# Performance work log

Measured on AMD Instinct MI355X. Metric: run time of the kernel, lower is better.

The kernel has to match this reference:

```python
import jax, jax.numpy as jnp
import numpy as np

# Module config (init_kwargs)
OUT_H, OUT_W = 7, 7
SPATIAL_SCALE = 0.25
SAMPLE_NUM = 2          # fixed sampling grid (sample_num > 0 branch of mmcv kernel)
ALIGNED = True
CLOCKWISE = False

B, C, H, W = 2, 256, 200, 200
R = 1000


def setup_inputs() -> dict:
    key = jax.random.key(0)
    k1, k2, k3, k4, k5, k6 = jax.random.split(key, 6)
    features = jax.random.normal(k1, (B, C, H, W), dtype=jnp.float32)
    # rois: (batch_index, cx, cy, w, h, angle) in input-image coordinates
    bidx = jax.random.randint(k2, (R,), 0, B).astype(jnp.float32)
    cx = jax.random.uniform(k3, (R,), minval=100.0, maxval=700.0)
    cy = jax.random.uniform(k4, (R,), minval=100.0, maxval=700.0)
    wh = jax.random.uniform(k5, (R, 2), minval=20.0, maxval=200.0)
    ang = jax.random.uniform(k6, (R,), minval=-np.pi, maxval=np.pi)
    rois = jnp.concatenate(
        [bidx[:, None], cx[:, None], cy[:, None], wh, ang[:, None]], axis=1
    ).astype(jnp.float32)
    return {"features": features, "rois": rois}


def _bilinear_gather(features, bidx, y, x):
    """features: [B,C,H,W]; bidx: [R] int; y,x: [R,P] float. Returns [R,P,C]."""
    Hf, Wf = features.shape[2], features.shape[3]
    valid = (y > -1.0) & (y < Hf) & (x > -1.0) & (x < Wf)
    y = jnp.maximum(y, 0.0)
    x = jnp.maximum(x, 0.0)
    yl = jnp.floor(y).astype(jnp.int32)
    xl = jnp.floor(x).astype(jnp.int32)
    ych = yl >= Hf - 1
    xch = xl >= Wf - 1
    yl = jnp.where(ych, Hf - 1, yl)
    yh = jnp.where(ych, Hf - 1, yl + 1)
    xl = jnp.where(xch, Wf - 1, xl)
    xh = jnp.where(xch, Wf - 1, xl + 1)
    ly = jnp.where(ych, 0.0, y - yl.astype(y.dtype))
    lx = jnp.where(xch, 0.0, x - xl.astype(x.dtype))
    hy, hx = 1.0 - ly, 1.0 - lx
    b = bidx[:, None]  # [R,1] broadcast against [R,P]
    v1 = features[b, :, yl, xl]  # [R,P,C]
    v2 = features[b, :, yl, xh]
    v3 = features[b, :, yh, xl]
    v4 = features[b, :, yh, xh]
    val = (hy * hx)[..., None] * v1 + (hy * lx)[..., None] * v2 \
        + (ly * hx)[..., None] * v3 + (ly * lx)[..., None] * v4
    return jnp.where(valid[..., None], val, 0.0)


def _roi_align_rotated(features, rois):
    g = SAMPLE_NUM
    offset = 0.5 if ALIGNED else 0.0
    bidx = rois[:, 0].astype(jnp.int32)
    cx = rois[:, 1] * SPATIAL_SCALE - offset
    cy = rois[:, 2] * SPATIAL_SCALE - offset
    rw = rois[:, 3] * SPATIAL_SCALE
    rh = rois[:, 4] * SPATIAL_SCALE
    theta = -rois[:, 5] if CLOCKWISE else rois[:, 5]
    if not ALIGNED:
        rw = jnp.maximum(rw, 1.0)
        rh = jnp.maximum(rh, 1.0)
    bin_h = rh / OUT_H
    bin_w = rw / OUT_W
    # sample offsets within roi frame, origin at roi center
    ph = jnp.arange(OUT_H, dtype=jnp.float32)
    pw = jnp.arange(OUT_W, dtype=jnp.float32)
    ig = (jnp.arange(g, dtype=jnp.float32) + 0.5) / g
    # yy: [R, OUT_H, g]; xx: [R, OUT_W, g]
    yy = -rh[:, None, None] / 2.0 + (ph[None, :, None] + ig[None, None, :]) * bin_h[:, None, None]
    xx = -rw[:, None, None] / 2.0 + (pw[None, :, None] + ig[None, None, :]) * bin_w[:, None, None]
    # broadcast to [R, OUT_H, OUT_W, g, g]
    yy5 = yy[:, :, None, :, None]
    xx5 = xx[:, None, :, None, :]
    sin_t = jnp.sin(theta)[:, None, None, None, None]
    cos_t = jnp.cos(theta)[:, None, None, None, None]
    x = yy5 * sin_t + xx5 * cos_t + cx[:, None, None, None, None]
    y = yy5 * cos_t - xx5 * sin_t + cy[:, None, None, None, None]
    P = OUT_H * OUT_W * g * g
    vals = _bilinear_gather(features, bidx, y.reshape(R, P), x.reshape(R, P))  # [R,P,C]
    vals = vals.reshape(R, OUT_H, OUT_W, g * g, C).mean(axis=3)  # [R,OUT_H,OUT_W,C]
    return jnp.transpose(vals, (0, 3, 1, 2))  # [R,C,OUT_H,OUT_W]


def reference(features, rois):
    return _roi_align_rotated(features, rois)
```

## Files before the change

kernel.cpp:

```cpp
#include <hip/hip_runtime.h>
#include <math.h>

#define OUT_H 7
#define OUT_W 7
#define GS 2
#define NBINS (OUT_H * OUT_W)
#define NSAMP (GS * GS)
#define NMETA (NBINS * NSAMP)
#define SPATIAL_SCALE 0.25f
#define B_ 2
#define C_ 256
#define H_ 200
#define W_ 200
#define R_ 1000
#define HW_ (H_ * W_)
#define NBH 25

typedef _Float16 half_t;
typedef __attribute__((ext_vector_type(4))) _Float16 half4;
typedef __attribute__((ext_vector_type(2))) _Float16 half2_t;


__global__ __launch_bounds__(256)
void nchw_to_nhwc_h(const float* __restrict__ in, half_t* __restrict__ out,
                    const float* __restrict__ rois, int* __restrict__ perm) {
    __shared__ float tile[64][65];

    __shared__ int cnt[8];
    __shared__ int novf, take;
    __shared__ unsigned char claimed[R_];
    __shared__ short ovf[R_];
    if (blockIdx.x == 0 && blockIdx.y == 0 && blockIdx.z == 0) {
        const int t0 = threadIdx.x;
        if (t0 < 8) cnt[t0] = 0;
        if (t0 == 0) { novf = 0; take = 0; }
        for (int t = t0; t < R_; t += 256) claimed[t] = 0;
        __syncthreads();
        for (int t = t0; t < R_; t += 256) {
            const float* roi = rois + t * 6;
            int   b   = (int)roi[0];
            float cyf = roi[2] * SPATIAL_SCALE;
            int q = (int)((cyf - 25.0f) * (4.0f / 150.0f));
            q = q < 0 ? 0 : (q > 3 ? 3 : q);
            int band = b * 4 + q;
            band = band < 0 ? 0 : (band > 7 ? 7 : band);
            int rank = atomicAdd(&cnt[band], 1);
            if (rank < R_ / 8) {
                int id = band + 8 * rank;
                perm[id] = t;
                claimed[id] = 1;
            } else {
                ovf[atomicAdd(&novf, 1)] = (short)t;
            }
        }
        __syncthreads();
        for (int t = t0; t < R_; t += 256) {
            if (!claimed[t]) perm[t] = (int)ovf[atomicAdd(&take, 1)];
        }
    }

    const int hw0 = blockIdx.x * 64;
    const int c0  = blockIdx.y * 64;
    const int b   = blockIdx.z;

    {
        const int tx = threadIdx.x & 63;
        const int ty = threadIdx.x >> 6;
        const float* ip = in + ((size_t)b * C_ + c0) * HW_ + hw0;
#pragma unroll
        for (int k = 0; k < 16; ++k)
            tile[ty + 4 * k][tx] = ip[(size_t)(ty + 4 * k) * HW_ + tx];
    }
    __syncthreads();
    {
        const int cp = threadIdx.x & 31;
        const int hr = threadIdx.x >> 5;
        half_t* op = out + ((size_t)b * HW_ + hw0) * C_ + c0;
#pragma unroll
        for (int k = 0; k < 8; ++k) {
            const int hw = hr + 8 * k;
            half2_t h;
            h[0] = (half_t)tile[2 * cp + 0][hw];
            h[1] = (half_t)tile[2 * cp + 1][hw];
            ((half2_t*)(op + (size_t)hw * C_))[cp] = h;
        }
    }
}

template<int B0, int NB>
__device__ __forceinline__ void gather_pass(
        const half4* __restrict__ fp,
        const int4* __restrict__ s_o, const float4* __restrict__ s_w,
        int wave, int lane, int tid,
        float (&obuf)[4][64][NBH], float* __restrict__ out_r) {

    for (int j = wave; j < NB; j += 8) {
        const int m = (B0 + j) * NSAMP;
        float ax = 0.0f, ay = 0.0f, az = 0.0f, aw = 0.0f;

#pragma unroll
        for (int sp = 0; sp < 2; ++sp) {
            const int4   oA = s_o[m + 2 * sp + 0];
            const int4   oB = s_o[m + 2 * sp + 1];
            const float4 wA = s_w[m + 2 * sp + 0];
            const float4 wB = s_w[m + 2 * sp + 1];

            const half4 vA0 = fp[oA.x + lane];
            const half4 vA1 = fp[oA.y + lane];
            const half4 vA2 = fp[oA.z + lane];
            const half4 vA3 = fp[oA.w + lane];
            const half4 vB0 = fp[oB.x + lane];
            const half4 vB1 = fp[oB.y + lane];
            const half4 vB2 = fp[oB.z + lane];
            const half4 vB3 = fp[oB.w + lane];

            ax = fmaf((float)vA0[0], wA.x, ax);
            ay = fmaf((float)vA0[1], wA.x, ay);
            az = fmaf((float)vA0[2], wA.x, az);
            aw = fmaf((float)vA0[3], wA.x, aw);
            ax = fmaf((float)vA1[0], wA.y, ax);
            ay = fmaf((float)vA1[1], wA.y, ay);
            az = fmaf((float)vA1[2], wA.y, az);
            aw = fmaf((float)vA1[3], wA.y, aw);
            ax = fmaf((float)vA2[0], wA.z, ax);
            ay = fmaf((float)vA2[1], wA.z, ay);
            az = fmaf((float)vA2[2], wA.z, az);
            aw = fmaf((float)vA2[3], wA.z, aw);
            ax = fmaf((float)vA3[0], wA.w, ax);
            ay = fmaf((float)vA3[1], wA.w, ay);
            az = fmaf((float)vA3[2], wA.w, az);
            aw = fmaf((float)vA3[3], wA.w, aw);

            ax = fmaf((float)vB0[0], wB.x, ax);
            ay = fmaf((float)vB0[1], wB.x, ay);
            az = fmaf((float)vB0[2], wB.x, az);
            aw = fmaf((float)vB0[3], wB.x, aw);
            ax = fmaf((float)vB1[0], wB.y, ax);
            ay = fmaf((float)vB1[1], wB.y, ay);
            az = fmaf((float)vB1[2], wB.y, az);
            aw = fmaf((float)vB1[3], wB.y, aw);
            ax = fmaf((float)vB2[0], wB.z, ax);
            ay = fmaf((float)vB2[1], wB.z, ay);
            az = fmaf((float)vB2[2], wB.z, az);
            aw = fmaf((float)vB2[3], wB.z, aw);
            ax = fmaf((float)vB3[0], wB.w, ax);
            ay = fmaf((float)vB3[1], wB.w, ay);
            az = fmaf((float)vB3[2], wB.w, az);
            aw = fmaf((float)vB3[3], wB.w, aw);
        }

        obuf[0][lane][j] = ax;
        obuf[1][lane][j] = ay;
        obuf[2][lane][j] = az;
        obuf[3][lane][j] = aw;
    }
    __syncthreads();

    const int E = C_ * NB;
#pragma unroll
    for (int i = 0; i < (E + 511) / 512; ++i) {
        const int e = tid + 512 * i;
        if (e < E) {
            const int c = e / NB;
            const int j = e - c * NB;
            out_r[(size_t)c * NBINS + B0 + j] = obuf[c & 3][c >> 2][j];
        }
    }
    __syncthreads();
}

__global__ __launch_bounds__(512, 8)
void gather_nhwc(const half_t* __restrict__ nhwc,
                 const float* __restrict__ rois,
                 const int* __restrict__ perm,
                 float* __restrict__ out) {
    __shared__ float obuf[4][64][NBH];
    __shared__ int4   s_o[NMETA];
    __shared__ float4 s_w[NMETA];

    const int r    = perm[blockIdx.x];
    const int tid  = threadIdx.x;
    const int wave = tid >> 6;
    const int lane = tid & 63;

    if (tid < NMETA) {
        const float* roi = rois + r * 6;
        const int   b     = (int)roi[0];
        const float cx    = roi[1] * SPATIAL_SCALE - 0.5f;
        const float cy    = roi[2] * SPATIAL_SCALE - 0.5f;
        const float rw    = roi[3] * SPATIAL_SCALE;
        const float rh    = roi[4] * SPATIAL_SCALE;
        const float theta = roi[5];
        const float bin_h = rh * (1.0f / OUT_H);
        const float bin_w = rw * (1.0f / OUT_W);
        float st, ct;
        __sincosf(theta, &st, &ct);

        const int bin = tid >> 2;
        const int s   = tid & 3;
        const int ph  = bin / OUT_W, pw = bin % OUT_W;
        const int iy  = s >> 1,      ix = s & 1;

        const float yy = -rh * 0.5f + ((float)ph + ((float)iy + 0.5f) * 0.5f) * bin_h;
        const float xx = -rw * 0.5f + ((float)pw + ((float)ix + 0.5f) * 0.5f) * bin_w;
        float x = yy * st + xx * ct + cx;
        float y = yy * ct - xx * st + cy;

        const bool valid = (y > -1.0f) && (y < (float)H_) &&
                           (x > -1.0f) && (x < (float)W_);
        y = fmaxf(y, 0.0f);
        x = fmaxf(x, 0.0f);
        int yl = (int)y, xl = (int)x;
        int yh; float ly;
        if (yl >= H_ - 1) { yl = H_ - 1; yh = H_ - 1; ly = 0.0f; }
        else              { yh = yl + 1; ly = y - (float)yl; }
        int xh; float lx;
        if (xl >= W_ - 1) { xl = W_ - 1; xh = W_ - 1; lx = 0.0f; }
        else              { xh = xl + 1; lx = x - (float)xl; }
        const float hy = 1.0f - ly, hx = 1.0f - lx;
        const float scale = valid ? (1.0f / NSAMP) : 0.0f;

        const int bplane = b * HW_;
        s_o[tid] = make_int4((bplane + yl * W_ + xl) * (C_ / 4),
                             (bplane + yl * W_ + xh) * (C_ / 4),
                             (bplane + yh * W_ + xl) * (C_ / 4),
                             (bplane + yh * W_ + xh) * (C_ / 4));
        s_w[tid] = make_float4(hy * hx * scale, hy * lx * scale,
                               ly * hx * scale, ly * lx * scale);
    }
    __syncthreads();

    const half4* __restrict__ fp = (const half4*)nhwc;
    float* out_r = out + (size_t)r * (C_ * NBINS);

    gather_pass< 0, 25>(fp, s_o, s_w, wave, lane, tid, obuf, out_r);
    gather_pass<25, 24>(fp, s_o, s_w, wave, lane, tid, obuf, out_r);
}


struct alignas(16) Samp {
    int o0, o1, o2, o3;
    float w0, w1, w2, w3;
};

__device__ __forceinline__ Samp compute_samp(const float* __restrict__ rois,
                                             int r, int ph, int pw, int s) {
    const float* roi = rois + r * 6;
    int   b     = (int)roi[0];
    float cx    = roi[1] * SPATIAL_SCALE - 0.5f;
    float cy    = roi[2] * SPATIAL_SCALE - 0.5f;
    float rw    = roi[3] * SPATIAL_SCALE;
    float rh    = roi[4] * SPATIAL_SCALE;
    float theta = roi[5];
    float bin_h = rh * (1.0f / OUT_H);
    float bin_w = rw * (1.0f / OUT_W);
    int iy = s / GS, ix = s % GS;
    float yy = -rh * 0.5f + ((float)ph + ((float)iy + 0.5f) * (1.0f / GS)) * bin_h;
    float xx = -rw * 0.5f + ((float)pw + ((float)ix + 0.5f) * (1.0f / GS)) * bin_w;
    float st = sinf(theta), ct = cosf(theta);
    float x = yy * st + xx * ct + cx;
    float y = yy * ct - xx * st + cy;
    bool valid = (y > -1.0f) && (y < (float)H_) && (x > -1.0f) && (x < (float)W_);
    y = fmaxf(y, 0.0f);
    x = fmaxf(x, 0.0f);
    int yl = (int)y;
    int xl = (int)x;
    int yh; float ly;
    if (yl >= H_ - 1) { yl = H_ - 1; yh = H_ - 1; ly = 0.0f; }
    else              { yh = yl + 1; ly = y - (float)yl; }
    int xh; float lx;
    if (xl >= W_ - 1) { xl = W_ - 1; xh = W_ - 1; lx = 0.0f; }
    else              { xh = xl + 1; lx = x - (float)xl; }
    float hy = 1.0f - ly, hx = 1.0f - lx;
    float scale = valid ? (1.0f / NSAMP) : 0.0f;
    Samp sp;
    int base = b * (C_ * H_ * W_);
    sp.o0 = base + yl * W_ + xl;
    sp.o1 = base + yl * W_ + xh;
    sp.o2 = base + yh * W_ + xl;
    sp.o3 = base + yh * W_ + xh;
    sp.w0 = hy * hx * scale;
    sp.w1 = hy * lx * scale;
    sp.w2 = ly * hx * scale;
    sp.w3 = ly * lx * scale;
    return sp;
}

__global__ __launch_bounds__(256)
void mono_kernel(const float* __restrict__ feat,
                 const float* __restrict__ rois,
                 float* __restrict__ out) {
    int tid = blockIdx.x * blockDim.x + threadIdx.x;
    if (tid >= R_ * C_ * NBINS) return;
    int bin = tid % NBINS;
    int rc  = tid / NBINS;
    int c   = rc % C_;
    int r   = rc / C_;
    int coff = c * (H_ * W_);
    float acc = 0.0f;
#pragma unroll
    for (int s = 0; s < NSAMP; ++s) {
        Samp t = compute_samp(rois, r, bin / OUT_W, bin % OUT_W, s);
        acc += t.w0 * feat[coff + t.o0];
        acc += t.w1 * feat[coff + t.o1];
        acc += t.w2 * feat[coff + t.o2];
        acc += t.w3 * feat[coff + t.o3];
    }
    out[tid] = acc;
}


extern "C" void kernel_launch(void* const* d_in, const int* in_sizes, int n_in,
                              void* d_out, int out_size, void* d_ws, size_t ws_size,
                              hipStream_t stream) {
    const float* feat = (const float*)d_in[0];
    const float* rois = (const float*)d_in[1];
    float* out = (float*)d_out;

    const size_t nhwc_bytes = (size_t)B_ * C_ * HW_ * sizeof(half_t);
    const size_t perm_bytes = (size_t)R_ * sizeof(int);

    if (ws_size >= nhwc_bytes + perm_bytes) {
        half_t* nhwc = (half_t*)d_ws;
        int*    perm = (int*)((char*)d_ws + nhwc_bytes);
        dim3 tgrid(HW_ / 64, C_ / 64, B_);
        nchw_to_nhwc_h<<<tgrid, 256, 0, stream>>>(feat, nhwc, rois, perm);
        gather_nhwc<<<R_, 512, 0, stream>>>(nhwc, rois, perm, out);
    } else {
        const int n_out = R_ * C_ * NBINS;
        mono_kernel<<<(n_out + 255) / 256, 256, 0, stream>>>(feat, rois, out);
    }
}
```

Baseline: 178.3 us.

## Split ROI gather into quarter blocks, use fma_mix, vectorize and swizzle transpose

The gather kernel now launches four 256-thread blocks per ROI, each covering 12 or 13 output bins, in place of one 512-thread block running two passes. This gives more and smaller blocks for scheduling. The inner accumulation uses inline v_fma_mix_f32 to multiply fp16 pairs directly into fp32 accumulators, with all 16 loads issued up front. The NCHW-to-NHWC transpose switches to 128-bit nontemporal loads, an XOR-swizzled shared tile, and 16-byte half8 stores. These changes add inline-asm dependence and recompute per-ROI metadata four times.

```diff
diff --git a/kernel.cpp b/kernel.cpp
--- a/kernel.cpp
+++ b/kernel.cpp
@@ -6,7 +6,6 @@
 #define GS 2
 #define NBINS (OUT_H * OUT_W)
 #define NSAMP (GS * GS)
-#define NMETA (NBINS * NSAMP)
 #define SPATIAL_SCALE 0.25f
 #define B_ 2
 #define C_ 256
@@ -14,17 +13,18 @@
 #define W_ 200
 #define R_ 1000
 #define HW_ (H_ * W_)
-#define NBH 25
+#define NBMAX 13
 
 typedef _Float16 half_t;
-typedef __attribute__((ext_vector_type(4))) _Float16 half4;
+typedef __attribute__((ext_vector_type(8))) _Float16 half8;
 typedef __attribute__((ext_vector_type(2))) _Float16 half2_t;
+typedef __attribute__((ext_vector_type(4))) float f32x4;
 
 
 __global__ __launch_bounds__(256)
 void nchw_to_nhwc_h(const float* __restrict__ in, half_t* __restrict__ out,
                     const float* __restrict__ rois, int* __restrict__ perm) {
-    __shared__ float tile[64][65];
+    __shared__ float tile[64][64];
 
     __shared__ int cnt[8];
     __shared__ int novf, take;
@@ -62,92 +62,99 @@
     const int hw0 = blockIdx.x * 64;
     const int c0  = blockIdx.y * 64;
     const int b   = blockIdx.z;
+    const int t   = threadIdx.x;
 
     {
-        const int tx = threadIdx.x & 63;
-        const int ty = threadIdx.x >> 6;
-        const float* ip = in + ((size_t)b * C_ + c0) * HW_ + hw0;
+        const f32x4* ip4 = (const f32x4*)(in + ((size_t)b * C_ + c0) * HW_ + hw0);
+        const int r = t >> 4;
+        const int q = t & 15;
 #pragma unroll
-        for (int k = 0; k < 16; ++k)
-            tile[ty + 4 * k][tx] = ip[(size_t)(ty + 4 * k) * HW_ + tx];
+        for (int k = 0; k < 4; ++k) {
+            const int c = r + 16 * k;
+            f32x4 v = __builtin_nontemporal_load(&ip4[(size_t)c * (HW_ / 4) + q]);
+            const int g = q ^ ((c ^ (c >> 3)) & 7);
+            ((f32x4*)tile)[c * 16 + g] = v;
+        }
     }
     __syncthreads();
     {
-        const int cp = threadIdx.x & 31;
-        const int hr = threadIdx.x >> 5;
-        half_t* op = out + ((size_t)b * HW_ + hw0) * C_ + c0;
+        const int cg = t & 7;
+        const int hb = t >> 3;
+        half_t* op = out + ((size_t)b * HW_ + hw0) * C_ + c0 + 8 * cg;
 #pragma unroll
-        for (int k = 0; k < 8; ++k) {
-            const int hw = hr + 8 * k;
-            half2_t h;
-            h[0] = (half_t)tile[2 * cp + 0][hw];
-            h[1] = (half_t)tile[2 * cp + 1][hw];
-            ((half2_t*)(op + (size_t)hw * C_))[cp] = h;
+        for (int i = 0; i < 2; ++i) {
+            const int hw = hb + 32 * i;
+            const int gh = hw >> 2, oh = hw & 3;
+            half8 h;
+#pragma unroll
+            for (int dc = 0; dc < 8; ++dc) {
+                const int c = 8 * cg + dc;
+                const float f = tile[c][4 * (gh ^ ((c ^ (c >> 3)) & 7)) + oh];
+                h[dc] = (half_t)f;
+            }
+            *(half8*)(op + (size_t)hw * C_) = h;
         }
     }
 }
 
-template<int B0, int NB>
-__device__ __forceinline__ void gather_pass(
-        const half4* __restrict__ fp,
+__device__ __forceinline__ void mix2(float& a0, float& a1,
+                                     unsigned int pair, float w) {
+    asm("v_fma_mix_f32 %0, %1, %2, %0 op_sel:[0,0,0] op_sel_hi:[1,0,0]"
+        : "+v"(a0) : "v"(pair), "v"(w));
+    asm("v_fma_mix_f32 %0, %1, %2, %0 op_sel:[1,0,0] op_sel_hi:[1,0,0]"
+        : "+v"(a1) : "v"(pair), "v"(w));
+}
+
+template<int NB>
+__device__ __forceinline__ void gather_body(
+        const uint2* __restrict__ fpu, int B0,
         const int4* __restrict__ s_o, const float4* __restrict__ s_w,
         int wave, int lane, int tid,
-        float (&obuf)[4][64][NBH], float* __restrict__ out_r) {
-
-    for (int j = wave; j < NB; j += 8) {
-        const int m = (B0 + j) * NSAMP;
+        float (&obuf)[4][64][NBMAX], float* __restrict__ out_r) {
+
+    for (int j = wave; j < NB; j += 4) {
+        const int m = j * NSAMP;
+        const int4   o0 = s_o[m + 0], o1 = s_o[m + 1], o2 = s_o[m + 2], o3 = s_o[m + 3];
+        const float4 w0 = s_w[m + 0], w1 = s_w[m + 1], w2 = s_w[m + 2], w3 = s_w[m + 3];
+
+        const uint2 t0  = fpu[o0.x + lane];
+        const uint2 t1  = fpu[o0.y + lane];
+        const uint2 t2  = fpu[o0.z + lane];
+        const uint2 t3  = fpu[o0.w + lane];
+        const uint2 t4  = fpu[o1.x + lane];
+        const uint2 t5  = fpu[o1.y + lane];
+        const uint2 t6  = fpu[o1.z + lane];
+        const uint2 t7  = fpu[o1.w + lane];
+        const uint2 t8  = fpu[o2.x + lane];
+        const uint2 t9  = fpu[o2.y + lane];
+        const uint2 t10 = fpu[o2.z + lane];
+        const uint2 t11 = fpu[o2.w + lane];
+        const uint2 t12 = fpu[o3.x + lane];
+        const uint2 t13 = fpu[o3.y + lane];
+        const uint2 t14 = fpu[o3.z + lane];
+        const uint2 t15 = fpu[o3.w + lane];
+
         float ax = 0.0f, ay = 0.0f, az = 0.0f, aw = 0.0f;
 
-#pragma unroll
-        for (int sp = 0; sp < 2; ++sp) {
-            const int4   oA = s_o[m + 2 * sp + 0];
-            const int4   oB = s_o[m + 2 * sp + 1];
-            const float4 wA = s_w[m + 2 * sp + 0];
-            const float4 wB = s_w[m + 2 * sp + 1];
-
-            const half4 vA0 = fp[oA.x + lane];
-            const half4 vA1 = fp[oA.y + lane];
-            const half4 vA2 = fp[oA.z + lane];
-            const half4 vA3 = fp[oA.w + lane];
-            const half4 vB0 = fp[oB.x + lane];
-            const half4 vB1 = fp[oB.y + lane];
-            const half4 vB2 = fp[oB.z + lane];
-            const half4 vB3 = fp[oB.w + lane];
-
-            ax = fmaf((float)vA0[0], wA.x, ax);
-            ay = fmaf((float)vA0[1], wA.x, ay);
-            az = fmaf((float)vA0[2], wA.x, az);
-            aw = fmaf((float)vA0[3], wA.x, aw);
-            ax = fmaf((float)vA1[0], wA.y, ax);
-            ay = fmaf((float)vA1[1], wA.y, ay);
-            az = fmaf((float)vA1[2], wA.y, az);
-            aw = fmaf((float)vA1[3], wA.y, aw);
-            ax = fmaf((float)vA2[0], wA.z, ax);
-            ay = fmaf((float)vA2[1], wA.z, ay);
-            az = fmaf((float)vA2[2], wA.z, az);
-            aw = fmaf((float)vA2[3], wA.z, aw);
-            ax = fmaf((float)vA3[0], wA.w, ax);
-            ay = fmaf((float)vA3[1], wA.w, ay);
-            az = fmaf((float)vA3[2], wA.w, az);
-            aw = fmaf((float)vA3[3], wA.w, aw);
-
-            ax = fmaf((float)vB0[0], wB.x, ax);
-            ay = fmaf((float)vB0[1], wB.x, ay);
-            az = fmaf((float)vB0[2], wB.x, az);
-            aw = fmaf((float)vB0[3], wB.x, aw);
-            ax = fmaf((float)vB1[0], wB.y, ax);
-            ay = fmaf((float)vB1[1], wB.y, ay);
-            az = fmaf((float)vB1[2], wB.y, az);
-            aw = fmaf((float)vB1[3], wB.y, aw);
-            ax = fmaf((float)vB2[0], wB.z, ax);
-            ay = fmaf((float)vB2[1], wB.z, ay);
-            az = fmaf((float)vB2[2], wB.z, az);
-            aw = fmaf((float)vB2[3], wB.z, aw);
-            ax = fmaf((float)vB3[0], wB.w, ax);
-            ay = fmaf((float)vB3[1], wB.w, ay);
-            az = fmaf((float)vB3[2], wB.w, az);
-            aw = fmaf((float)vB3[3], wB.w, aw);
-        }
+        mix2(ax, ay, t0.x,  w0.x); mix2(az, aw, t0.y,  w0.x);
+        mix2(ax, ay, t1.x,  w0.y); mix2(az, aw, t1.y,  w0.y);
+        mix2(ax, ay, t2.x,  w0.z); mix2(az, aw, t2.y,  w0.z);
+        mix2(ax, ay, t3.x,  w0.w); mix2(az, aw, t3.y,  w0.w);
+
+        mix2(ax, ay, t4.x,  w1.x); mix2(az, aw, t4.y,  w1.x);
+        mix2(ax, ay, t5.x,  w1.y); mix2(az, aw, t5.y,  w1.y);
+        mix2(ax, ay, t6.x,  w1.z); mix2(az, aw, t6.y,  w1.z);
+        mix2(ax, ay, t7.x,  w1.w); mix2(az, aw, t7.y,  w1.w);
+
+        mix2(ax, ay, t8.x,  w2.x); mix2(az, aw, t8.y,  w2.x);
+        mix2(ax, ay, t9.x,  w2.y); mix2(az, aw, t9.y,  w2.y);
+        mix2(ax, ay, t10.x, w2.z); mix2(az, aw, t10.y, w2.z);
+        mix2(ax, ay, t11.x, w2.w); mix2(az, aw, t11.y, w2.w);
+
+        mix2(ax, ay, t12.x, w3.x); mix2(az, aw, t12.y, w3.x);
+        mix2(ax, ay, t13.x, w3.y); mix2(az, aw, t13.y, w3.y);
+        mix2(ax, ay, t14.x, w3.z); mix2(az, aw, t14.y, w3.z);
+        mix2(ax, ay, t15.x, w3.w); mix2(az, aw, t15.y, w3.w);
 
         obuf[0][lane][j] = ax;
         obuf[1][lane][j] = ay;
@@ -157,33 +164,34 @@
     __syncthreads();
 
     const int E = C_ * NB;
-#pragma unroll
-    for (int i = 0; i < (E + 511) / 512; ++i) {
-        const int e = tid + 512 * i;
-        if (e < E) {
-            const int c = e / NB;
-            const int j = e - c * NB;
-            out_r[(size_t)c * NBINS + B0 + j] = obuf[c & 3][c >> 2][j];
-        }
-    }
-    __syncthreads();
-}
-
-__global__ __launch_bounds__(512, 8)
+    for (int e = tid; e < E; e += 256) {
+        const int c = e / NB;
+        const int j = e - c * NB;
+        out_r[(size_t)c * NBINS + B0 + j] = obuf[c & 3][c >> 2][j];
+    }
+}
+
+__global__ __launch_bounds__(256, 6)
 void gather_nhwc(const half_t* __restrict__ nhwc,
                  const float* __restrict__ rois,
                  const int* __restrict__ perm,
                  float* __restrict__ out) {
-    __shared__ float obuf[4][64][NBH];
-    __shared__ int4   s_o[NMETA];
-    __shared__ float4 s_w[NMETA];
-
-    const int r    = perm[blockIdx.x];
+    __shared__ float  obuf[4][64][NBMAX];
+    __shared__ int4   s_o[NBMAX * NSAMP];
+    __shared__ float4 s_w[NBMAX * NSAMP];
+
+    const int bid  = blockIdx.x;
+    const int q    = bid / 1000;
+    const int slot = bid - q * 1000;
+    const int r    = perm[slot];
+    const int NB   = (q == 3) ? 13 : 12;
+    const int B0   = 12 * q;
+
     const int tid  = threadIdx.x;
     const int wave = tid >> 6;
     const int lane = tid & 63;
 
-    if (tid < NMETA) {
+    if (tid < NB * NSAMP) {
         const float* roi = rois + r * 6;
         const int   b     = (int)roi[0];
         const float cx    = roi[1] * SPATIAL_SCALE - 0.5f;
@@ -196,7 +204,7 @@
         float st, ct;
         __sincosf(theta, &st, &ct);
 
-        const int bin = tid >> 2;
+        const int bin = B0 + (tid >> 2);
         const int s   = tid & 3;
         const int ph  = bin / OUT_W, pw = bin % OUT_W;
         const int iy  = s >> 1,      ix = s & 1;
@@ -230,11 +238,11 @@
     }
     __syncthreads();
 
-    const half4* __restrict__ fp = (const half4*)nhwc;
+    const uint2* __restrict__ fpu = (const uint2*)nhwc;
     float* out_r = out + (size_t)r * (C_ * NBINS);
 
-    gather_pass< 0, 25>(fp, s_o, s_w, wave, lane, tid, obuf, out_r);
-    gather_pass<25, 24>(fp, s_o, s_w, wave, lane, tid, obuf, out_r);
+    if (q == 3) gather_body<13>(fpu, B0, s_o, s_w, wave, lane, tid, obuf, out_r);
+    else        gather_body<12>(fpu, B0, s_o, s_w, wave, lane, tid, obuf, out_r);
 }
 
 
@@ -325,7 +333,7 @@
         int*    perm = (int*)((char*)d_ws + nhwc_bytes);
         dim3 tgrid(HW_ / 64, C_ / 64, B_);
         nchw_to_nhwc_h<<<tgrid, 256, 0, stream>>>(feat, nhwc, rois, perm);
-        gather_nhwc<<<R_, 512, 0, stream>>>(nhwc, rois, perm, out);
+        gather_nhwc<<<4 * R_, 256, 0, stream>>>(nhwc, rois, perm, out);
     } else {
         const int n_out = R_ * C_ * NBINS;
         mono_kernel<<<(n_out + 255) / 256, 256, 0, stream>>>(feat, rois, out);
```

New measurement: 174.6 us. -2.1%, faster.
